# Kernel optimization log

Measured on AMD Instinct MI355X. Metric: run time of the kernel, lower is better.

## Reference

```python
import jax, jax.numpy as jnp
import numpy as np

TOP_K = 2
NOISE_STDDEV = 1.0


def setup_inputs() -> dict:
    key = jax.random.key(0)
    k1, k2, k3, k4 = jax.random.split(key, 4)
    N, D, E = 16384, 2048, 64
    x = jax.random.normal(k1, (N, D), dtype=jnp.float32)
    W_gate = jax.random.normal(k2, (E, D), dtype=jnp.float32) * (1.0 / np.sqrt(D))
    W_noise = jax.random.normal(k3, (E, D), dtype=jnp.float32) * (1.0 / np.sqrt(D))
    noise = jax.random.normal(k4, (N, E), dtype=jnp.float32)
    return {"x": x, "W_gate": W_gate, "W_noise": W_noise, "noise": noise}


def reference(x, W_gate, W_noise, noise):
    # clean gating logits: [N, E]
    clean_logits = jnp.einsum("nd,ed->ne", x, W_gate)
    # noise scale via softplus of second projection (training mode)
    noise_scale = jax.nn.softplus(jnp.einsum("nd,ed->ne", x, W_noise))
    noisy_logits = clean_logits + noise_scale * noise * NOISE_STDDEV
    # top-k selection then softmax over the k selected logits
    top_k_logits, top_k_indices = jax.lax.top_k(noisy_logits, TOP_K)
    combined_weights = jax.nn.softmax(top_k_logits, axis=-1)
    return (combined_weights, top_k_indices, clean_logits)
```

## Files before the change

### kernel.cpp

```cpp
#include <hip/hip_runtime.h>
#include <math.h>


constexpr int NROWS = 16384;
constexpr int DDIM  = 2048;
constexpr int EDIM  = 64;
constexpr int BM    = 64;
constexpr int NKS   = 64;
constexpr int LSTR  = 132;
constexpr int IDX_OFF   = NROWS * 2;
constexpr int CLEAN_OFF = NROWS * 4;
constexpr size_t WPACK = 262144;
constexpr int BUFSZ = 24576;
constexpr int NBUF  = 4;

typedef _Float16 f16x8 __attribute__((ext_vector_type(8)));
typedef float    f32x4 __attribute__((ext_vector_type(4)));

__device__ __forceinline__ float softplus_f(float z) {
    return fmaxf(z, 0.0f) + log1pf(expf(-fabsf(z)));
}

__device__ __forceinline__ void gload16(const void* g, void* l) {
    __builtin_amdgcn_global_load_lds(
        (const __attribute__((address_space(1))) unsigned int*)g,
        (__attribute__((address_space(3))) unsigned int*)l, 16, 0, 0);
}

__global__ __launch_bounds__(256) void split_w_kernel(
    const float* __restrict__ Wg, const float* __restrict__ Wn,
    _Float16* __restrict__ wh, _Float16* __restrict__ wl)
{
    const int t    = blockIdx.x * 256 + threadIdx.x;
    const int grp  = t >> 6;
    const int lane = t & 63;
    const int kc   = grp >> 3;
    const int cg   = (grp >> 1) & 3;
    const int cf   = grp & 1;
    const int col  = cg * 32 + cf * 16 + (lane & 15);
    const int k0   = kc * 32 + (lane >> 4) * 8;
    const float* src = (col < 64) ? &Wg[(size_t)col * DDIM + k0]
                                  : &Wn[(size_t)(col - 64) * DDIM + k0];
    const float4 v0 = *reinterpret_cast<const float4*>(src);
    const float4 v1 = *reinterpret_cast<const float4*>(src + 4);
    float vv[8] = {v0.x, v0.y, v0.z, v0.w, v1.x, v1.y, v1.z, v1.w};
    union { _Float16 h[8]; uint4 u; } hh, ll;
    #pragma unroll
    for (int j = 0; j < 8; ++j) {
        hh.h[j] = (_Float16)vv[j];
        ll.h[j] = (_Float16)((vv[j] - (float)hh.h[j]) * 2048.0f);
    }
    const size_t off = (size_t)grp * 512 + lane * 8;
    *reinterpret_cast<uint4*>(&wh[off]) = hh.u;
    *reinterpret_cast<uint4*>(&wl[off]) = ll.u;
}

__device__ __forceinline__ void split8(const float4 a, const float4 b, f16x8& h, f16x8& l) {
    const float v[8] = {a.x, a.y, a.z, a.w, b.x, b.y, b.z, b.w};
    #pragma unroll
    for (int j = 0; j < 8; ++j) {
        const _Float16 hh = (_Float16)v[j];
        h[j] = hh;
        l[j] = (_Float16)((v[j] - (float)hh) * 2048.0f);
    }
}

__global__ __launch_bounds__(512, 1) void gating_mfma_kernel(
    const float* __restrict__ x,
    const float* __restrict__ noise,
    const _Float16* __restrict__ whp,
    const _Float16* __restrict__ wlp,
    float* __restrict__ out)
{
    extern __shared__ __align__(16) unsigned char smem[];

    const int tid = threadIdx.x;
    const int row_base = blockIdx.x * BM;
    const int lane = tid & 63;
    const int wid  = tid >> 6;
    const int g    = (lane >> 4) & 3;
    const int idx  = lane & 15;
    const int rg   = wid >> 2;
    const int cg   = wid & 3;

    const int sr  = tid >> 3;
    const int sq  = tid & 7;
    const int sq2 = sq ^ (sr & 7);
    const float* xsrc = x + (size_t)(row_base + sr) * DDIM + sq2 * 4;
    const char* bhsrc = (const char*)whp + tid * 16;
    const char* blsrc = (const char*)wlp + tid * 16;

    int aoff[2][2];
    #pragma unroll
    for (int rf = 0; rf < 2; ++rf) {
        const int row = rg * 32 + rf * 16 + idx;
        #pragma unroll
        for (int s = 0; s < 2; ++s)
            aoff[rf][s] = row * 128 + (((g * 2 + s) ^ (row & 7)) << 4);
    }
    int bhoff[2], bloff[2];
    #pragma unroll
    for (int cf = 0; cf < 2; ++cf) {
        bhoff[cf] = 8192  + (cg * 2 + cf) * 1024 + lane * 16;
        bloff[cf] = 16384 + (cg * 2 + cf) * 1024 + lane * 16;
    }

    f32x4 accm[2][2], accc[2][2];
    #pragma unroll
    for (int rf = 0; rf < 2; ++rf)
        #pragma unroll
        for (int cf = 0; cf < 2; ++cf) { accm[rf][cf] = (f32x4)0.0f; accc[rf][cf] = (f32x4)0.0f; }

    auto stage = [&](int u) {
        const int b = (u & (NBUF - 1)) * BUFSZ;
        gload16(xsrc + u * 32,                 smem + b + tid * 16);
        gload16(bhsrc + (size_t)u * 8192,      smem + b + 8192 + tid * 16);
        gload16(blsrc + (size_t)u * 8192,      smem + b + 16384 + tid * 16);
    };

    auto computeStep = [&](int b) {
        const float4 a00 = *reinterpret_cast<const float4*>(&smem[b + aoff[0][0]]);
        const float4 a01 = *reinterpret_cast<const float4*>(&smem[b + aoff[0][1]]);
        const float4 a10 = *reinterpret_cast<const float4*>(&smem[b + aoff[1][0]]);
        const float4 a11 = *reinterpret_cast<const float4*>(&smem[b + aoff[1][1]]);
        const f16x8 Bh0 = *reinterpret_cast<const f16x8*>(&smem[b + bhoff[0]]);
        const f16x8 Bh1 = *reinterpret_cast<const f16x8*>(&smem[b + bhoff[1]]);
        const f16x8 Bl0 = *reinterpret_cast<const f16x8*>(&smem[b + bloff[0]]);
        const f16x8 Bl1 = *reinterpret_cast<const f16x8*>(&smem[b + bloff[1]]);

        f16x8 Ah0, Al0, Ah1, Al1;
        split8(a00, a01, Ah0, Al0);
        split8(a10, a11, Ah1, Al1);

        accm[0][0] = __builtin_amdgcn_mfma_f32_16x16x32_f16(Ah0, Bh0, accm[0][0], 0, 0, 0);
        accm[0][1] = __builtin_amdgcn_mfma_f32_16x16x32_f16(Ah0, Bh1, accm[0][1], 0, 0, 0);
        accm[1][0] = __builtin_amdgcn_mfma_f32_16x16x32_f16(Ah1, Bh0, accm[1][0], 0, 0, 0);
        accm[1][1] = __builtin_amdgcn_mfma_f32_16x16x32_f16(Ah1, Bh1, accm[1][1], 0, 0, 0);
        accc[0][0] = __builtin_amdgcn_mfma_f32_16x16x32_f16(Al0, Bh0, accc[0][0], 0, 0, 0);
        accc[0][1] = __builtin_amdgcn_mfma_f32_16x16x32_f16(Al0, Bh1, accc[0][1], 0, 0, 0);
        accc[1][0] = __builtin_amdgcn_mfma_f32_16x16x32_f16(Al1, Bh0, accc[1][0], 0, 0, 0);
        accc[1][1] = __builtin_amdgcn_mfma_f32_16x16x32_f16(Al1, Bh1, accc[1][1], 0, 0, 0);
        accc[0][0] = __builtin_amdgcn_mfma_f32_16x16x32_f16(Ah0, Bl0, accc[0][0], 0, 0, 0);
        accc[0][1] = __builtin_amdgcn_mfma_f32_16x16x32_f16(Ah0, Bl1, accc[0][1], 0, 0, 0);
        accc[1][0] = __builtin_amdgcn_mfma_f32_16x16x32_f16(Ah1, Bl0, accc[1][0], 0, 0, 0);
        accc[1][1] = __builtin_amdgcn_mfma_f32_16x16x32_f16(Ah1, Bl1, accc[1][1], 0, 0, 0);
    };

    stage(0);
    stage(1);

    for (int t = 0; t < NKS - 2; ++t) {
        stage(t + 2);
        asm volatile("s_waitcnt vmcnt(6)" ::: "memory");
        __builtin_amdgcn_s_barrier();
        __builtin_amdgcn_sched_barrier(0);
        computeStep((t & (NBUF - 1)) * BUFSZ);
    }
    asm volatile("s_waitcnt vmcnt(3)" ::: "memory");
    __builtin_amdgcn_s_barrier();
    __builtin_amdgcn_sched_barrier(0);
    computeStep(((NKS - 2) & (NBUF - 1)) * BUFSZ);
    asm volatile("s_waitcnt vmcnt(0)" ::: "memory");
    __builtin_amdgcn_s_barrier();
    __builtin_amdgcn_sched_barrier(0);
    computeStep(((NKS - 1) & (NBUF - 1)) * BUFSZ);

    __builtin_amdgcn_s_barrier();

    float* L = reinterpret_cast<float*>(smem);
    #pragma unroll
    for (int rf = 0; rf < 2; ++rf)
        #pragma unroll
        for (int cf = 0; cf < 2; ++cf) {
            const int col = cg * 32 + cf * 16 + idx;
            #pragma unroll
            for (int q = 0; q < 4; ++q) {
                const int lrow = rg * 32 + rf * 16 + g * 4 + q;
                L[lrow * LSTR + col] = accm[rf][cf][q] + accc[rf][cf][q] * 4.8828125e-4f;
            }
        }
    __syncthreads();

    {
        const int row = tid >> 3;
        const int j   = tid & 7;
        const int e0  = j * 8;
        const int grow = row_base + row;

        const float4 c0 = *reinterpret_cast<const float4*>(&L[row * LSTR + e0]);
        const float4 c1 = *reinterpret_cast<const float4*>(&L[row * LSTR + e0 + 4]);
        const float4 s0 = *reinterpret_cast<const float4*>(&L[row * LSTR + 64 + e0]);
        const float4 s1 = *reinterpret_cast<const float4*>(&L[row * LSTR + 64 + e0 + 4]);
        *reinterpret_cast<float4*>(&out[CLEAN_OFF + (size_t)grow * EDIM + e0])     = c0;
        *reinterpret_cast<float4*>(&out[CLEAN_OFF + (size_t)grow * EDIM + e0 + 4]) = c1;

        const float4 z0 = *reinterpret_cast<const float4*>(&noise[(size_t)grow * EDIM + e0]);
        const float4 z1 = *reinterpret_cast<const float4*>(&noise[(size_t)grow * EDIM + e0 + 4]);

        float nv[8];
        nv[0] = fmaf(softplus_f(s0.x), z0.x, c0.x);
        nv[1] = fmaf(softplus_f(s0.y), z0.y, c0.y);
        nv[2] = fmaf(softplus_f(s0.z), z0.z, c0.z);
        nv[3] = fmaf(softplus_f(s0.w), z0.w, c0.w);
        nv[4] = fmaf(softplus_f(s1.x), z1.x, c1.x);
        nv[5] = fmaf(softplus_f(s1.y), z1.y, c1.y);
        nv[6] = fmaf(softplus_f(s1.z), z1.z, c1.z);
        nv[7] = fmaf(softplus_f(s1.w), z1.w, c1.w);

        float v0 = nv[0], v1 = -INFINITY;
        int   i0 = e0,    i1 = -1;
        #pragma unroll
        for (int m = 1; m < 8; ++m) {
            const float v = nv[m]; const int e = e0 + m;
            if (v > v0)      { v1 = v0; i1 = i0; v0 = v; i0 = e; }
            else if (v > v1) { v1 = v;  i1 = e; }
        }
        #pragma unroll
        for (int d = 1; d < 8; d <<= 1) {
            const float ov0 = __shfl_xor(v0, d); const int oi0 = __shfl_xor(i0, d);
            const float ov1 = __shfl_xor(v1, d); const int oi1 = __shfl_xor(i1, d);
            const bool aFirst = (v0 > ov0) || (v0 == ov0 && i0 < oi0);
            float n0, n1; int ni0, ni1;
            if (aFirst) {
                n0 = v0; ni0 = i0;
                const bool s = (v1 > ov0) || (v1 == ov0 && i1 < oi0);
                n1 = s ? v1 : ov0; ni1 = s ? i1 : oi0;
            } else {
                n0 = ov0; ni0 = oi0;
                const bool s = (ov1 > v0) || (ov1 == v0 && oi1 < i0);
                n1 = s ? ov1 : v0; ni1 = s ? oi1 : i0;
            }
            v0 = n0; i0 = ni0; v1 = n1; i1 = ni1;
        }
        if (j == 0) {
            const float ex = expf(v1 - v0);
            const float w0 = 1.0f / (1.0f + ex);
            const float w1 = 1.0f - w0;
            out[(size_t)grow * 2 + 0] = w0;
            out[(size_t)grow * 2 + 1] = w1;
            out[IDX_OFF + (size_t)grow * 2 + 0] = (float)i0;
            out[IDX_OFF + (size_t)grow * 2 + 1] = (float)i1;
        }
    }
}

extern "C" void kernel_launch(void* const* d_in, const int* in_sizes, int n_in,
                              void* d_out, int out_size, void* d_ws, size_t ws_size,
                              hipStream_t stream) {
    const float* x     = (const float*)d_in[0];
    const float* Wg    = (const float*)d_in[1];
    const float* Wn    = (const float*)d_in[2];
    const float* noise = (const float*)d_in[3];
    float* out = (float*)d_out;

    _Float16* wh = (_Float16*)d_ws;
    _Float16* wl = wh + WPACK;

    split_w_kernel<<<dim3(128), dim3(256), 0, stream>>>(Wg, Wn, wh, wl);
    gating_mfma_kernel<<<dim3(NROWS / BM), dim3(512), NBUF * BUFSZ, stream>>>(x, noise, wh, wl, out);
}
```

Baseline: 53.92 us.

## Double the K-step per pipeline stage and restructure to three-buffer prefetch

Each pipeline stage now loads two K-slices (64 columns of x and two weight slabs), so there is one barrier per two compute steps. The ring drops from four 24KB buffers to three 48KB buffers. The next stage's loads are now issued after the barrier rather than before the wait, which is what makes three buffers safe. This halves the barrier and waitcnt overhead per unit of work, at the cost of more LDS per block (144KB), which may lower occupancy.

```diff
diff --git a/kernel.cpp b/kernel.cpp
--- a/kernel.cpp
+++ b/kernel.cpp
@@ -6,13 +6,13 @@
 constexpr int DDIM  = 2048;
 constexpr int EDIM  = 64;
 constexpr int BM    = 64;
-constexpr int NKS   = 64;
+constexpr int NIT   = 32;
 constexpr int LSTR  = 132;
 constexpr int IDX_OFF   = NROWS * 2;
 constexpr int CLEAN_OFF = NROWS * 4;
 constexpr size_t WPACK = 262144;
-constexpr int BUFSZ = 24576;
-constexpr int NBUF  = 4;
+constexpr int BUFSZ = 49152;
+constexpr int NBUF  = 3;
 
 typedef _Float16 f16x8 __attribute__((ext_vector_type(8)));
 typedef float    f32x4 __attribute__((ext_vector_type(4)));
@@ -90,20 +90,24 @@
     const char* bhsrc = (const char*)whp + tid * 16;
     const char* blsrc = (const char*)wlp + tid * 16;
 
-    int aoff[2][2];
-    #pragma unroll
-    for (int rf = 0; rf < 2; ++rf) {
-        const int row = rg * 32 + rf * 16 + idx;
-        #pragma unroll
-        for (int s = 0; s < 2; ++s)
-            aoff[rf][s] = row * 128 + (((g * 2 + s) ^ (row & 7)) << 4);
-    }
-    int bhoff[2], bloff[2];
-    #pragma unroll
-    for (int cf = 0; cf < 2; ++cf) {
-        bhoff[cf] = 8192  + (cg * 2 + cf) * 1024 + lane * 16;
-        bloff[cf] = 16384 + (cg * 2 + cf) * 1024 + lane * 16;
-    }
+    int aoff[2][2][2];
+    #pragma unroll
+    for (int ks = 0; ks < 2; ++ks)
+        #pragma unroll
+        for (int rf = 0; rf < 2; ++rf) {
+            const int row = rg * 32 + rf * 16 + idx;
+            #pragma unroll
+            for (int j = 0; j < 2; ++j)
+                aoff[ks][rf][j] = ks * 8192 + row * 128 + (((g * 2 + j) ^ (row & 7)) << 4);
+        }
+    int bhoff[2][2], bloff[2][2];
+    #pragma unroll
+    for (int ks = 0; ks < 2; ++ks)
+        #pragma unroll
+        for (int cf = 0; cf < 2; ++cf) {
+            bhoff[ks][cf] = 16384 + ks * 8192 + (cg * 2 + cf) * 1024 + lane * 16;
+            bloff[ks][cf] = 32768 + ks * 8192 + (cg * 2 + cf) * 1024 + lane * 16;
+        }
 
     f32x4 accm[2][2], accc[2][2];
     #pragma unroll
@@ -112,21 +116,24 @@
         for (int cf = 0; cf < 2; ++cf) { accm[rf][cf] = (f32x4)0.0f; accc[rf][cf] = (f32x4)0.0f; }
 
     auto stage = [&](int u) {
-        const int b = (u & (NBUF - 1)) * BUFSZ;
-        gload16(xsrc + u * 32,                 smem + b + tid * 16);
-        gload16(bhsrc + (size_t)u * 8192,      smem + b + 8192 + tid * 16);
-        gload16(blsrc + (size_t)u * 8192,      smem + b + 16384 + tid * 16);
+        const int b = (u % NBUF) * BUFSZ;
+        gload16(xsrc + u * 64,                      smem + b + tid * 16);
+        gload16(xsrc + u * 64 + 32,                 smem + b + 8192 + tid * 16);
+        gload16(bhsrc + (size_t)(2 * u) * 8192,     smem + b + 16384 + tid * 16);
+        gload16(bhsrc + (size_t)(2 * u + 1) * 8192, smem + b + 24576 + tid * 16);
+        gload16(blsrc + (size_t)(2 * u) * 8192,     smem + b + 32768 + tid * 16);
+        gload16(blsrc + (size_t)(2 * u + 1) * 8192, smem + b + 40960 + tid * 16);
     };
 
-    auto computeStep = [&](int b) {
-        const float4 a00 = *reinterpret_cast<const float4*>(&smem[b + aoff[0][0]]);
-        const float4 a01 = *reinterpret_cast<const float4*>(&smem[b + aoff[0][1]]);
-        const float4 a10 = *reinterpret_cast<const float4*>(&smem[b + aoff[1][0]]);
-        const float4 a11 = *reinterpret_cast<const float4*>(&smem[b + aoff[1][1]]);
-        const f16x8 Bh0 = *reinterpret_cast<const f16x8*>(&smem[b + bhoff[0]]);
-        const f16x8 Bh1 = *reinterpret_cast<const f16x8*>(&smem[b + bhoff[1]]);
-        const f16x8 Bl0 = *reinterpret_cast<const f16x8*>(&smem[b + bloff[0]]);
-        const f16x8 Bl1 = *reinterpret_cast<const f16x8*>(&smem[b + bloff[1]]);
+    auto computeStep = [&](int b, int ks) {
+        const float4 a00 = *reinterpret_cast<const float4*>(&smem[b + aoff[ks][0][0]]);
+        const float4 a01 = *reinterpret_cast<const float4*>(&smem[b + aoff[ks][0][1]]);
+        const float4 a10 = *reinterpret_cast<const float4*>(&smem[b + aoff[ks][1][0]]);
+        const float4 a11 = *reinterpret_cast<const float4*>(&smem[b + aoff[ks][1][1]]);
+        const f16x8 Bh0 = *reinterpret_cast<const f16x8*>(&smem[b + bhoff[ks][0]]);
+        const f16x8 Bh1 = *reinterpret_cast<const f16x8*>(&smem[b + bhoff[ks][1]]);
+        const f16x8 Bl0 = *reinterpret_cast<const f16x8*>(&smem[b + bloff[ks][0]]);
+        const f16x8 Bl1 = *reinterpret_cast<const f16x8*>(&smem[b + bloff[ks][1]]);
 
         f16x8 Ah0, Al0, Ah1, Al1;
         split8(a00, a01, Ah0, Al0);
@@ -149,21 +156,20 @@
     stage(0);
     stage(1);
 
-    for (int t = 0; t < NKS - 2; ++t) {
-        stage(t + 2);
-        asm volatile("s_waitcnt vmcnt(6)" ::: "memory");
+    int rbase = 0;
+    for (int t = 0; t < NIT; ++t) {
+        if (t < NIT - 1) {
+            asm volatile("s_waitcnt vmcnt(6)" ::: "memory");
+        } else {
+            asm volatile("s_waitcnt vmcnt(0)" ::: "memory");
+        }
         __builtin_amdgcn_s_barrier();
+        if (t < NIT - 2) stage(t + 2);
         __builtin_amdgcn_sched_barrier(0);
-        computeStep((t & (NBUF - 1)) * BUFSZ);
-    }
-    asm volatile("s_waitcnt vmcnt(3)" ::: "memory");
-    __builtin_amdgcn_s_barrier();
-    __builtin_amdgcn_sched_barrier(0);
-    computeStep(((NKS - 2) & (NBUF - 1)) * BUFSZ);
-    asm volatile("s_waitcnt vmcnt(0)" ::: "memory");
-    __builtin_amdgcn_s_barrier();
-    __builtin_amdgcn_sched_barrier(0);
-    computeStep(((NKS - 1) & (NBUF - 1)) * BUFSZ);
+        computeStep(rbase, 0);
+        computeStep(rbase, 1);
+        rbase += BUFSZ; if (rbase == NBUF * BUFSZ) rbase = 0;
+    }
 
     __builtin_amdgcn_s_barrier();
 
```

After: 67.95 us. 26.0% more time.

## Halve row tile to 32 and run two 256-thread blocks per CU with triple buffering

Applied to the files above, without the earlier changes.

Shrinks each workgroup from 64 rows and 8 waves to 32 rows and 4 waves, with launch bounds allowing two blocks per CU. The loop becomes a 3-buffer ring that issues the next stage after the barrier. The aim is to let two independent blocks overlap their load and compute phases and to spread the epilogue across more blocks. In exchange, each block still streams the full packed fp16 weight pair, so total weight traffic doubles.

```diff
diff --git a/kernel.cpp b/kernel.cpp
--- a/kernel.cpp
+++ b/kernel.cpp
@@ -5,14 +5,14 @@
 constexpr int NROWS = 16384;
 constexpr int DDIM  = 2048;
 constexpr int EDIM  = 64;
-constexpr int BM    = 64;
+constexpr int BM    = 32;
 constexpr int NKS   = 64;
 constexpr int LSTR  = 132;
 constexpr int IDX_OFF   = NROWS * 2;
 constexpr int CLEAN_OFF = NROWS * 4;
 constexpr size_t WPACK = 262144;
-constexpr int BUFSZ = 24576;
-constexpr int NBUF  = 4;
+constexpr int BUFSZ = 20480;
+constexpr int NBUF  = 3;
 
 typedef _Float16 f16x8 __attribute__((ext_vector_type(8)));
 typedef float    f32x4 __attribute__((ext_vector_type(4)));
@@ -65,7 +65,7 @@
     }
 }
 
-__global__ __launch_bounds__(512, 1) void gating_mfma_kernel(
+__global__ __launch_bounds__(256, 2) void gating_mfma_kernel(
     const float* __restrict__ x,
     const float* __restrict__ noise,
     const _Float16* __restrict__ whp,
@@ -77,11 +77,9 @@
     const int tid = threadIdx.x;
     const int row_base = blockIdx.x * BM;
     const int lane = tid & 63;
-    const int wid  = tid >> 6;
+    const int cg   = tid >> 6;
     const int g    = (lane >> 4) & 3;
     const int idx  = lane & 15;
-    const int rg   = wid >> 2;
-    const int cg   = wid & 3;
 
     const int sr  = tid >> 3;
     const int sq  = tid & 7;
@@ -93,16 +91,16 @@
     int aoff[2][2];
     #pragma unroll
     for (int rf = 0; rf < 2; ++rf) {
-        const int row = rg * 32 + rf * 16 + idx;
-        #pragma unroll
-        for (int s = 0; s < 2; ++s)
-            aoff[rf][s] = row * 128 + (((g * 2 + s) ^ (row & 7)) << 4);
+        const int row = rf * 16 + idx;
+        #pragma unroll
+        for (int j = 0; j < 2; ++j)
+            aoff[rf][j] = row * 128 + (((g * 2 + j) ^ (row & 7)) << 4);
     }
     int bhoff[2], bloff[2];
     #pragma unroll
     for (int cf = 0; cf < 2; ++cf) {
-        bhoff[cf] = 8192  + (cg * 2 + cf) * 1024 + lane * 16;
-        bloff[cf] = 16384 + (cg * 2 + cf) * 1024 + lane * 16;
+        bhoff[cf] = 4096  + (cg * 2 + cf) * 1024 + lane * 16;
+        bloff[cf] = 12288 + (cg * 2 + cf) * 1024 + lane * 16;
     }
 
     f32x4 accm[2][2], accc[2][2];
@@ -111,11 +109,12 @@
         #pragma unroll
         for (int cf = 0; cf < 2; ++cf) { accm[rf][cf] = (f32x4)0.0f; accc[rf][cf] = (f32x4)0.0f; }
 
-    auto stage = [&](int u) {
-        const int b = (u & (NBUF - 1)) * BUFSZ;
-        gload16(xsrc + u * 32,                 smem + b + tid * 16);
-        gload16(bhsrc + (size_t)u * 8192,      smem + b + 8192 + tid * 16);
-        gload16(blsrc + (size_t)u * 8192,      smem + b + 16384 + tid * 16);
+    auto stage = [&](int u, int b) {
+        gload16(xsrc + u * 32,                        smem + b + tid * 16);
+        gload16(bhsrc + (size_t)u * 8192,             smem + b + 4096  + tid * 16);
+        gload16(bhsrc + (size_t)u * 8192 + 4096,      smem + b + 8192  + tid * 16);
+        gload16(blsrc + (size_t)u * 8192,             smem + b + 12288 + tid * 16);
+        gload16(blsrc + (size_t)u * 8192 + 4096,      smem + b + 16384 + tid * 16);
     };
 
     auto computeStep = [&](int b) {
@@ -146,24 +145,23 @@
         accc[1][1] = __builtin_amdgcn_mfma_f32_16x16x32_f16(Ah1, Bl1, accc[1][1], 0, 0, 0);
     };
 
-    stage(0);
-    stage(1);
-
-    for (int t = 0; t < NKS - 2; ++t) {
-        stage(t + 2);
-        asm volatile("s_waitcnt vmcnt(6)" ::: "memory");
+    stage(0, 0);
+    stage(1, BUFSZ);
+
+    int rbase = 0, wbase = 2 * BUFSZ;
+    for (int t = 0; t < NKS; ++t) {
+        if (t < NKS - 1) {
+            asm volatile("s_waitcnt vmcnt(5)" ::: "memory");
+        } else {
+            asm volatile("s_waitcnt vmcnt(0)" ::: "memory");
+        }
         __builtin_amdgcn_s_barrier();
+        if (t < NKS - 2) stage(t + 2, wbase);
         __builtin_amdgcn_sched_barrier(0);
-        computeStep((t & (NBUF - 1)) * BUFSZ);
-    }
-    asm volatile("s_waitcnt vmcnt(3)" ::: "memory");
-    __builtin_amdgcn_s_barrier();
-    __builtin_amdgcn_sched_barrier(0);
-    computeStep(((NKS - 2) & (NBUF - 1)) * BUFSZ);
-    asm volatile("s_waitcnt vmcnt(0)" ::: "memory");
-    __builtin_amdgcn_s_barrier();
-    __builtin_amdgcn_sched_barrier(0);
-    computeStep(((NKS - 1) & (NBUF - 1)) * BUFSZ);
+        computeStep(rbase);
+        rbase += BUFSZ; if (rbase == NBUF * BUFSZ) rbase = 0;
+        wbase += BUFSZ; if (wbase == NBUF * BUFSZ) wbase = 0;
+    }
 
     __builtin_amdgcn_s_barrier();
 
@@ -175,7 +173,7 @@
             const int col = cg * 32 + cf * 16 + idx;
             #pragma unroll
             for (int q = 0; q < 4; ++q) {
-                const int lrow = rg * 32 + rf * 16 + g * 4 + q;
+                const int lrow = rf * 16 + g * 4 + q;
                 L[lrow * LSTR + col] = accm[rf][cf][q] + accc[rf][cf][q] * 4.8828125e-4f;
             }
         }
@@ -257,5 +255,5 @@
     _Float16* wl = wh + WPACK;
 
     split_w_kernel<<<dim3(128), dim3(256), 0, stream>>>(Wg, Wn, wh, wl);
-    gating_mfma_kernel<<<dim3(NROWS / BM), dim3(512), NBUF * BUFSZ, stream>>>(x, noise, wh, wl, out);
-}
+    gating_mfma_kernel<<<dim3(NROWS / BM), dim3(256), NBUF * BUFSZ, stream>>>(x, noise, wh, wl, out);
+}
```

Measured after the change: 65.04 us. 1.21x slower.

## Split-K GEMM with 128-row tiles and separate reduce/top-k kernel

Applied to the files above, without the earlier changes.

The gating GEMM now uses 128-row tiles so each block reuses its weight tiles across twice as many rows, and it splits K into two halves so the grid is 256 blocks. Partial logits go to a workspace buffer, and a new kernel sums the two halves and runs the softplus/noise/top-k epilogue. This cuts how often the packed weights are reloaded per row, but adds a partial-sum round-trip through global memory and an extra kernel launch.

```diff
diff --git a/kernel.cpp b/kernel.cpp
--- a/kernel.cpp
+++ b/kernel.cpp
@@ -5,14 +5,13 @@
 constexpr int NROWS = 16384;
 constexpr int DDIM  = 2048;
 constexpr int EDIM  = 64;
-constexpr int BM    = 64;
-constexpr int NKS   = 64;
-constexpr int LSTR  = 132;
 constexpr int IDX_OFF   = NROWS * 2;
 constexpr int CLEAN_OFF = NROWS * 4;
 constexpr size_t WPACK = 262144;
-constexpr int BUFSZ = 24576;
-constexpr int NBUF  = 4;
+constexpr int BMAIN = 128;
+constexpr int NKS2  = 32;
+constexpr int BUFSZ2 = 32768;
+constexpr int NBUF2  = 4;
 
 typedef _Float16 f16x8 __attribute__((ext_vector_type(8)));
 typedef float    f32x4 __attribute__((ext_vector_type(4)));
@@ -65,182 +64,198 @@
     }
 }
 
-__global__ __launch_bounds__(512, 1) void gating_mfma_kernel(
+__global__ __launch_bounds__(512, 1) void gemm_part_kernel(
     const float* __restrict__ x,
-    const float* __restrict__ noise,
     const _Float16* __restrict__ whp,
     const _Float16* __restrict__ wlp,
-    float* __restrict__ out)
+    float* __restrict__ pbuf)
 {
     extern __shared__ __align__(16) unsigned char smem[];
 
-    const int tid = threadIdx.x;
-    const int row_base = blockIdx.x * BM;
+    const int tid  = threadIdx.x;
     const int lane = tid & 63;
     const int wid  = tid >> 6;
+    const int rg   = wid >> 2;
+    const int cg   = wid & 3;
     const int g    = (lane >> 4) & 3;
     const int idx  = lane & 15;
-    const int rg   = wid >> 2;
-    const int cg   = wid & 3;
+    const int kh   = blockIdx.x >> 7;
+    const int rt   = blockIdx.x & 127;
+    const int row_base = rt * BMAIN;
 
     const int sr  = tid >> 3;
     const int sq  = tid & 7;
     const int sq2 = sq ^ (sr & 7);
-    const float* xsrc = x + (size_t)(row_base + sr) * DDIM + sq2 * 4;
-    const char* bhsrc = (const char*)whp + tid * 16;
-    const char* blsrc = (const char*)wlp + tid * 16;
-
-    int aoff[2][2];
-    #pragma unroll
-    for (int rf = 0; rf < 2; ++rf) {
-        const int row = rg * 32 + rf * 16 + idx;
-        #pragma unroll
-        for (int s = 0; s < 2; ++s)
-            aoff[rf][s] = row * 128 + (((g * 2 + s) ^ (row & 7)) << 4);
+    const float* xs0 = x + (size_t)(row_base + sr) * DDIM + kh * 1024 + sq2 * 4;
+    const float* xs1 = xs0 + (size_t)64 * DDIM;
+    const char* bhsrc = (const char*)whp + (size_t)kh * 524288 + tid * 16;
+    const char* blsrc = (const char*)wlp + (size_t)kh * 524288 + tid * 16;
+
+    const char* bh2 = (const char*)whp + (size_t)kh * 262144 + tid * 16;
+    const char* bl2 = (const char*)wlp + (size_t)kh * 262144 + tid * 16;
+
+    int aoff[4][2];
+    #pragma unroll
+    for (int rf = 0; rf < 4; ++rf) {
+        const int r6 = rf * 16 + idx;
+        #pragma unroll
+        for (int j = 0; j < 2; ++j)
+            aoff[rf][j] = rg * 8192 + r6 * 128 + (((2 * g + j) ^ (r6 & 7)) << 4);
     }
     int bhoff[2], bloff[2];
     #pragma unroll
     for (int cf = 0; cf < 2; ++cf) {
-        bhoff[cf] = 8192  + (cg * 2 + cf) * 1024 + lane * 16;
-        bloff[cf] = 16384 + (cg * 2 + cf) * 1024 + lane * 16;
-    }
-
-    f32x4 accm[2][2], accc[2][2];
-    #pragma unroll
-    for (int rf = 0; rf < 2; ++rf)
+        bhoff[cf] = 16384 + (cg * 2 + cf) * 1024 + lane * 16;
+        bloff[cf] = 24576 + (cg * 2 + cf) * 1024 + lane * 16;
+    }
+
+    f32x4 accm[4][2], accc[4][2];
+    #pragma unroll
+    for (int rf = 0; rf < 4; ++rf)
         #pragma unroll
         for (int cf = 0; cf < 2; ++cf) { accm[rf][cf] = (f32x4)0.0f; accc[rf][cf] = (f32x4)0.0f; }
 
     auto stage = [&](int u) {
-        const int b = (u & (NBUF - 1)) * BUFSZ;
-        gload16(xsrc + u * 32,                 smem + b + tid * 16);
-        gload16(bhsrc + (size_t)u * 8192,      smem + b + 8192 + tid * 16);
-        gload16(blsrc + (size_t)u * 8192,      smem + b + 16384 + tid * 16);
+        const int b = (u & (NBUF2 - 1)) * BUFSZ2;
+        gload16(xs0 + u * 32,            smem + b + tid * 16);
+        gload16(xs1 + u * 32,            smem + b + 8192 + tid * 16);
+        gload16(bh2 + (size_t)u * 8192,  smem + b + 16384 + tid * 16);
+        gload16(bl2 + (size_t)u * 8192,  smem + b + 24576 + tid * 16);
     };
 
-    auto computeStep = [&](int b) {
-        const float4 a00 = *reinterpret_cast<const float4*>(&smem[b + aoff[0][0]]);
-        const float4 a01 = *reinterpret_cast<const float4*>(&smem[b + aoff[0][1]]);
-        const float4 a10 = *reinterpret_cast<const float4*>(&smem[b + aoff[1][0]]);
-        const float4 a11 = *reinterpret_cast<const float4*>(&smem[b + aoff[1][1]]);
+    auto compute = [&](int t) {
+        const int b = (t & (NBUF2 - 1)) * BUFSZ2;
+        f16x8 Ah[4], Al[4];
+        #pragma unroll
+        for (int rf = 0; rf < 4; ++rf) {
+            const float4 a0 = *reinterpret_cast<const float4*>(&smem[b + aoff[rf][0]]);
+            const float4 a1 = *reinterpret_cast<const float4*>(&smem[b + aoff[rf][1]]);
+            split8(a0, a1, Ah[rf], Al[rf]);
+        }
         const f16x8 Bh0 = *reinterpret_cast<const f16x8*>(&smem[b + bhoff[0]]);
         const f16x8 Bh1 = *reinterpret_cast<const f16x8*>(&smem[b + bhoff[1]]);
         const f16x8 Bl0 = *reinterpret_cast<const f16x8*>(&smem[b + bloff[0]]);
         const f16x8 Bl1 = *reinterpret_cast<const f16x8*>(&smem[b + bloff[1]]);
-
-        f16x8 Ah0, Al0, Ah1, Al1;
-        split8(a00, a01, Ah0, Al0);
-        split8(a10, a11, Ah1, Al1);
-
-        accm[0][0] = __builtin_amdgcn_mfma_f32_16x16x32_f16(Ah0, Bh0, accm[0][0], 0, 0, 0);
-        accm[0][1] = __builtin_amdgcn_mfma_f32_16x16x32_f16(Ah0, Bh1, accm[0][1], 0, 0, 0);
-        accm[1][0] = __builtin_amdgcn_mfma_f32_16x16x32_f16(Ah1, Bh0, accm[1][0], 0, 0, 0);
-        accm[1][1] = __builtin_amdgcn_mfma_f32_16x16x32_f16(Ah1, Bh1, accm[1][1], 0, 0, 0);
-        accc[0][0] = __builtin_amdgcn_mfma_f32_16x16x32_f16(Al0, Bh0, accc[0][0], 0, 0, 0);
-        accc[0][1] = __builtin_amdgcn_mfma_f32_16x16x32_f16(Al0, Bh1, accc[0][1], 0, 0, 0);
-        accc[1][0] = __builtin_amdgcn_mfma_f32_16x16x32_f16(Al1, Bh0, accc[1][0], 0, 0, 0);
-        accc[1][1] = __builtin_amdgcn_mfma_f32_16x16x32_f16(Al1, Bh1, accc[1][1], 0, 0, 0);
-        accc[0][0] = __builtin_amdgcn_mfma_f32_16x16x32_f16(Ah0, Bl0, accc[0][0], 0, 0, 0);
-        accc[0][1] = __builtin_amdgcn_mfma_f32_16x16x32_f16(Ah0, Bl1, accc[0][1], 0, 0, 0);
-        accc[1][0] = __builtin_amdgcn_mfma_f32_16x16x32_f16(Ah1, Bl0, accc[1][0], 0, 0, 0);
-        accc[1][1] = __builtin_amdgcn_mfma_f32_16x16x32_f16(Ah1, Bl1, accc[1][1], 0, 0, 0);
+        #pragma unroll
+        for (int rf = 0; rf < 4; ++rf) {
+            accm[rf][0] = __builtin_amdgcn_mfma_f32_16x16x32_f16(Ah[rf], Bh0, accm[rf][0], 0, 0, 0);
+            accm[rf][1] = __builtin_amdgcn_mfma_f32_16x16x32_f16(Ah[rf], Bh1, accm[rf][1], 0, 0, 0);
+            accc[rf][0] = __builtin_amdgcn_mfma_f32_16x16x32_f16(Al[rf], Bh0, accc[rf][0], 0, 0, 0);
+            accc[rf][1] = __builtin_amdgcn_mfma_f32_16x16x32_f16(Al[rf], Bh1, accc[rf][1], 0, 0, 0);
+            accc[rf][0] = __builtin_amdgcn_mfma_f32_16x16x32_f16(Ah[rf], Bl0, accc[rf][0], 0, 0, 0);
+            accc[rf][1] = __builtin_amdgcn_mfma_f32_16x16x32_f16(Ah[rf], Bl1, accc[rf][1], 0, 0, 0);
+        }
     };
 
     stage(0);
     stage(1);
-
-    for (int t = 0; t < NKS - 2; ++t) {
+    for (int t = 0; t < NKS2 - 2; ++t) {
         stage(t + 2);
-        asm volatile("s_waitcnt vmcnt(6)" ::: "memory");
+        asm volatile("s_waitcnt vmcnt(8)" ::: "memory");
         __builtin_amdgcn_s_barrier();
         __builtin_amdgcn_sched_barrier(0);
-        computeStep((t & (NBUF - 1)) * BUFSZ);
-    }
-    asm volatile("s_waitcnt vmcnt(3)" ::: "memory");
+        compute(t);
+    }
+    asm volatile("s_waitcnt vmcnt(4)" ::: "memory");
     __builtin_amdgcn_s_barrier();
     __builtin_amdgcn_sched_barrier(0);
-    computeStep(((NKS - 2) & (NBUF - 1)) * BUFSZ);
+    compute(NKS2 - 2);
     asm volatile("s_waitcnt vmcnt(0)" ::: "memory");
     __builtin_amdgcn_s_barrier();
     __builtin_amdgcn_sched_barrier(0);
-    computeStep(((NKS - 1) & (NBUF - 1)) * BUFSZ);
-
-    __builtin_amdgcn_s_barrier();
-
-    float* L = reinterpret_cast<float*>(smem);
-    #pragma unroll
-    for (int rf = 0; rf < 2; ++rf)
+    compute(NKS2 - 1);
+
+    float* dst = pbuf + (size_t)kh * NROWS * 128;
+    #pragma unroll
+    for (int rf = 0; rf < 4; ++rf)
         #pragma unroll
         for (int cf = 0; cf < 2; ++cf) {
             const int col = cg * 32 + cf * 16 + idx;
             #pragma unroll
             for (int q = 0; q < 4; ++q) {
-                const int lrow = rg * 32 + rf * 16 + g * 4 + q;
-                L[lrow * LSTR + col] = accm[rf][cf][q] + accc[rf][cf][q] * 4.8828125e-4f;
+                const int lrow = rg * 64 + rf * 16 + g * 4 + q;
+                dst[(size_t)(row_base + lrow) * 128 + col] =
+                    accm[rf][cf][q] + accc[rf][cf][q] * 4.8828125e-4f;
             }
         }
-    __syncthreads();
-
-    {
-        const int row = tid >> 3;
-        const int j   = tid & 7;
-        const int e0  = j * 8;
-        const int grow = row_base + row;
-
-        const float4 c0 = *reinterpret_cast<const float4*>(&L[row * LSTR + e0]);
-        const float4 c1 = *reinterpret_cast<const float4*>(&L[row * LSTR + e0 + 4]);
-        const float4 s0 = *reinterpret_cast<const float4*>(&L[row * LSTR + 64 + e0]);
-        const float4 s1 = *reinterpret_cast<const float4*>(&L[row * LSTR + 64 + e0 + 4]);
-        *reinterpret_cast<float4*>(&out[CLEAN_OFF + (size_t)grow * EDIM + e0])     = c0;
-        *reinterpret_cast<float4*>(&out[CLEAN_OFF + (size_t)grow * EDIM + e0 + 4]) = c1;
-
-        const float4 z0 = *reinterpret_cast<const float4*>(&noise[(size_t)grow * EDIM + e0]);
-        const float4 z1 = *reinterpret_cast<const float4*>(&noise[(size_t)grow * EDIM + e0 + 4]);
-
-        float nv[8];
-        nv[0] = fmaf(softplus_f(s0.x), z0.x, c0.x);
-        nv[1] = fmaf(softplus_f(s0.y), z0.y, c0.y);
-        nv[2] = fmaf(softplus_f(s0.z), z0.z, c0.z);
-        nv[3] = fmaf(softplus_f(s0.w), z0.w, c0.w);
-        nv[4] = fmaf(softplus_f(s1.x), z1.x, c1.x);
-        nv[5] = fmaf(softplus_f(s1.y), z1.y, c1.y);
-        nv[6] = fmaf(softplus_f(s1.z), z1.z, c1.z);
-        nv[7] = fmaf(softplus_f(s1.w), z1.w, c1.w);
-
-        float v0 = nv[0], v1 = -INFINITY;
-        int   i0 = e0,    i1 = -1;
-        #pragma unroll
-        for (int m = 1; m < 8; ++m) {
-            const float v = nv[m]; const int e = e0 + m;
-            if (v > v0)      { v1 = v0; i1 = i0; v0 = v; i0 = e; }
-            else if (v > v1) { v1 = v;  i1 = e; }
-        }
-        #pragma unroll
-        for (int d = 1; d < 8; d <<= 1) {
-            const float ov0 = __shfl_xor(v0, d); const int oi0 = __shfl_xor(i0, d);
-            const float ov1 = __shfl_xor(v1, d); const int oi1 = __shfl_xor(i1, d);
-            const bool aFirst = (v0 > ov0) || (v0 == ov0 && i0 < oi0);
-            float n0, n1; int ni0, ni1;
-            if (aFirst) {
-                n0 = v0; ni0 = i0;
-                const bool s = (v1 > ov0) || (v1 == ov0 && i1 < oi0);
-                n1 = s ? v1 : ov0; ni1 = s ? i1 : oi0;
-            } else {
-                n0 = ov0; ni0 = oi0;
-                const bool s = (ov1 > v0) || (ov1 == v0 && oi1 < i0);
-                n1 = s ? ov1 : v0; ni1 = s ? oi1 : i0;
-            }
-            v0 = n0; i0 = ni0; v1 = n1; i1 = ni1;
-        }
-        if (j == 0) {
-            const float ex = expf(v1 - v0);
-            const float w0 = 1.0f / (1.0f + ex);
-            const float w1 = 1.0f - w0;
-            out[(size_t)grow * 2 + 0] = w0;
-            out[(size_t)grow * 2 + 1] = w1;
-            out[IDX_OFF + (size_t)grow * 2 + 0] = (float)i0;
-            out[IDX_OFF + (size_t)grow * 2 + 1] = (float)i1;
-        }
+}
+
+__global__ __launch_bounds__(256) void reduce_topk_kernel(
+    const float* __restrict__ pbuf,
+    const float* __restrict__ noise,
+    float* __restrict__ out)
+{
+    const int tid = threadIdx.x;
+    const int row = tid >> 3;
+    const int j   = tid & 7;
+    const int e0  = j * 8;
+    const int grow = blockIdx.x * 32 + row;
+
+    const float* p0 = pbuf + (size_t)grow * 128;
+    const float* p1 = pbuf + (size_t)(NROWS + grow) * 128;
+
+    float4 c0 = *reinterpret_cast<const float4*>(&p0[e0]);
+    float4 c1 = *reinterpret_cast<const float4*>(&p0[e0 + 4]);
+    float4 s0 = *reinterpret_cast<const float4*>(&p0[64 + e0]);
+    float4 s1 = *reinterpret_cast<const float4*>(&p0[64 + e0 + 4]);
+    const float4 d0 = *reinterpret_cast<const float4*>(&p1[e0]);
+    const float4 d1 = *reinterpret_cast<const float4*>(&p1[e0 + 4]);
+    const float4 t0 = *reinterpret_cast<const float4*>(&p1[64 + e0]);
+    const float4 t1 = *reinterpret_cast<const float4*>(&p1[64 + e0 + 4]);
+    c0.x += d0.x; c0.y += d0.y; c0.z += d0.z; c0.w += d0.w;
+    c1.x += d1.x; c1.y += d1.y; c1.z += d1.z; c1.w += d1.w;
+    s0.x += t0.x; s0.y += t0.y; s0.z += t0.z; s0.w += t0.w;
+    s1.x += t1.x; s1.y += t1.y; s1.z += t1.z; s1.w += t1.w;
+
+    *reinterpret_cast<float4*>(&out[CLEAN_OFF + (size_t)grow * EDIM + e0])     = c0;
+    *reinterpret_cast<float4*>(&out[CLEAN_OFF + (size_t)grow * EDIM + e0 + 4]) = c1;
+
+    const float4 z0 = *reinterpret_cast<const float4*>(&noise[(size_t)grow * EDIM + e0]);
+    const float4 z1 = *reinterpret_cast<const float4*>(&noise[(size_t)grow * EDIM + e0 + 4]);
+
+    float nv[8];
+    nv[0] = fmaf(softplus_f(s0.x), z0.x, c0.x);
+    nv[1] = fmaf(softplus_f(s0.y), z0.y, c0.y);
+    nv[2] = fmaf(softplus_f(s0.z), z0.z, c0.z);
+    nv[3] = fmaf(softplus_f(s0.w), z0.w, c0.w);
+    nv[4] = fmaf(softplus_f(s1.x), z1.x, c1.x);
+    nv[5] = fmaf(softplus_f(s1.y), z1.y, c1.y);
+    nv[6] = fmaf(softplus_f(s1.z), z1.z, c1.z);
+    nv[7] = fmaf(softplus_f(s1.w), z1.w, c1.w);
+
+    float v0 = nv[0], v1 = -INFINITY;
+    int   i0 = e0,    i1 = -1;
+    #pragma unroll
+    for (int m = 1; m < 8; ++m) {
+        const float v = nv[m]; const int e = e0 + m;
+        if (v > v0)      { v1 = v0; i1 = i0; v0 = v; i0 = e; }
+        else if (v > v1) { v1 = v;  i1 = e; }
+    }
+    #pragma unroll
+    for (int d = 1; d < 8; d <<= 1) {
+        const float ov0 = __shfl_xor(v0, d); const int oi0 = __shfl_xor(i0, d);
+        const float ov1 = __shfl_xor(v1, d); const int oi1 = __shfl_xor(i1, d);
+        const bool aFirst = (v0 > ov0) || (v0 == ov0 && i0 < oi0);
+        float n0, n1; int ni0, ni1;
+        if (aFirst) {
+            n0 = v0; ni0 = i0;
+            const bool s = (v1 > ov0) || (v1 == ov0 && i1 < oi0);
+            n1 = s ? v1 : ov0; ni1 = s ? i1 : oi0;
+        } else {
+            n0 = ov0; ni0 = oi0;
+            const bool s = (ov1 > v0) || (ov1 == v0 && oi1 < i0);
+            n1 = s ? ov1 : v0; ni1 = s ? oi1 : i0;
+        }
+        v0 = n0; i0 = ni0; v1 = n1; i1 = ni1;
+    }
+    if (j == 0) {
+        const float ex = expf(v1 - v0);
+        const float w0 = 1.0f / (1.0f + ex);
+        const float w1 = 1.0f - w0;
+        out[(size_t)grow * 2 + 0] = w0;
+        out[(size_t)grow * 2 + 1] = w1;
+        out[IDX_OFF + (size_t)grow * 2 + 0] = (float)i0;
+        out[IDX_OFF + (size_t)grow * 2 + 1] = (float)i1;
     }
 }
 
@@ -255,7 +270,9 @@
 
     _Float16* wh = (_Float16*)d_ws;
     _Float16* wl = wh + WPACK;
+    float* pbuf  = (float*)((char*)d_ws + (1 << 20));
 
     split_w_kernel<<<dim3(128), dim3(256), 0, stream>>>(Wg, Wn, wh, wl);
-    gating_mfma_kernel<<<dim3(NROWS / BM), dim3(512), NBUF * BUFSZ, stream>>>(x, noise, wh, wl, out);
-}
+    gemm_part_kernel<<<dim3(256), dim3(512), NBUF2 * BUFSZ2, stream>>>(x, wh, wl, pbuf);
+    reduce_topk_kernel<<<dim3(NROWS / 32), dim3(256), 0, stream>>>(pbuf, noise, out);
+}
```

New measurement: 52.96 us. About the same (-1.8%).
